# Performance work log

Measured on AMD Instinct MI355X. Metric: run time of the kernel, lower is better.

Reference implementation:

```python
import jax, jax.numpy as jnp
import numpy as np

LMAX, MMAX = 6, 2
C, COUT = 128, 128
M_SIZE = [LMAX - m + 1 for m in range(MMAX + 1)]  # [7, 6, 5]
LN_EPS = 1e-5


def _perm():
    # l-primary layout (input): for l in 0..lmax, m in -min(l,mmax)..min(l,mmax)
    lp = [(l, m) for l in range(LMAX + 1) for m in range(-min(l, MMAX), min(l, MMAX) + 1)]
    # m-primary layout (CoefficientMapping.to_m): m=0 block, then per m: real(+m) block, imag(-m) block
    mp = [(l, 0) for l in range(LMAX + 1)]
    for m in range(1, MMAX + 1):
        mp += [(l, m) for l in range(m, LMAX + 1)]
        mp += [(l, -m) for l in range(m, LMAX + 1)]
    return np.array([lp.index(t) for t in mp], dtype=np.int32)

PERM = _perm()  # length 29


def setup_inputs() -> dict:
    key = jax.random.key(0)
    ks = jax.random.split(key, 8)
    E = 30000
    num_coeff = sum(2 * min(l, MMAX) + 1 for l in range(LMAX + 1))  # 29
    rad_out = C * sum(M_SIZE)  # 2304 = num_channels_rad
    s = 0.02
    return {
        "x_emb": jax.random.normal(ks[0], (E, num_coeff, C), jnp.float32),
        "x_edge": jax.random.normal(ks[1], (E, C), jnp.float32),
        # RadialFunction: Linear(C,C)+LN+SiLU, Linear(C, rad_out)
        "rad_w1": jax.random.normal(ks[2], (C, C), jnp.float32) * s,
        "rad_b1": jnp.zeros((C,), jnp.float32),
        "rad_g": jnp.ones((C,), jnp.float32),
        "rad_beta": jnp.zeros((C,), jnp.float32),
        "rad_w2": jax.random.normal(ks[3], (rad_out, C), jnp.float32) * s,
        "rad_b2": jnp.ones((rad_out,), jnp.float32),  # gate ~1 so signal survives
        # fc_m0: Linear(7*C, COUT*7, bias=True)
        "w_m0": jax.random.normal(ks[4], (M_SIZE[0] * COUT, M_SIZE[0] * C), jnp.float32) * s,
        "b_m0": jnp.zeros((M_SIZE[0] * COUT,), jnp.float32),
        # SO2_m_Convolution fc for m=1,2: Linear(msz*C, 2*COUT*msz, bias=False)
        "w_m1": jax.random.normal(ks[5], (2 * COUT * M_SIZE[1], M_SIZE[1] * C), jnp.float32) * s,
        "w_m2": jax.random.normal(ks[6], (2 * COUT * M_SIZE[2], M_SIZE[2] * C), jnp.float32) * s,
    }


def reference(x_emb, x_edge, rad_w1, rad_b1, rad_g, rad_beta, rad_w2, rad_b2,
              w_m0, b_m0, w_m1, w_m2):
    E = x_emb.shape[0]
    # _m_primary: permute coefficients from l-primary to m-primary layout
    xm = x_emb[:, PERM, :]  # (E, 29, C)

    # RadialFunction: Linear + LayerNorm + SiLU + Linear
    h = x_edge @ rad_w1.T + rad_b1
    mu = jnp.mean(h, axis=-1, keepdims=True)
    var = jnp.var(h, axis=-1, keepdims=True)
    h = (h - mu) * jax.lax.rsqrt(var + LN_EPS) * rad_g + rad_beta
    h = jax.nn.silu(h)
    rad = h @ rad_w2.T + rad_b2  # (E, 2304)

    # m = 0
    m0 = M_SIZE[0]
    x0 = xm[:, :m0, :].reshape(E, m0 * C)
    x0 = x0 * rad[:, : m0 * C]
    x0 = x0 @ w_m0.T + b_m0  # (E, m0*COUT)
    outs = [x0.reshape(E, m0, COUT)]

    offset, offr = m0, m0 * C
    for msz, w in zip(M_SIZE[1:], (w_m1, w_m2)):
        # (E, 2, msz*C): row 0 = real(+m) coeffs, row 1 = imag(-m) coeffs
        x_m = xm[:, offset:offset + 2 * msz, :].reshape(E, 2, msz * C)
        x_m = x_m * rad[:, offr:offr + msz * C][:, None, :]
        y = jnp.einsum('eki,oi->eko', x_m, w)  # (E, 2, 2*COUT*msz)
        half = w.shape[0] // 2
        y_r, y_i = y[..., :half], y[..., half:]
        out_r = y_r[:, 0:1] - y_i[:, 1:2]
        out_i = y_r[:, 1:2] + y_i[:, 0:1]
        outs.append(jnp.concatenate([out_r, out_i], axis=1).reshape(E, 2 * msz, COUT))
        offset += 2 * msz
        offr += msz * C

    return jnp.concatenate(outs, axis=1)  # (E, 29, COUT), m-primary layout
```

## Files before the change

kernel.cpp:

```cpp
#include <hip/hip_runtime.h>
#include <stdint.h>

typedef unsigned short u16;
typedef __attribute__((ext_vector_type(8))) short short8;
typedef __attribute__((ext_vector_type(8))) u16 u16x8;
typedef __attribute__((ext_vector_type(4))) u16 u16x4;
typedef __attribute__((ext_vector_type(4))) float f32x4;

#define E_TOT 30000
#define TL    3712

__constant__ int d_PERM[29] = {0,2,6,11,16,21,26, 3,7,12,17,22,27, 1,5,10,15,20,25,
                               8,13,18,23,28, 4,9,14,19,24};
__constant__ int d_RINV[18][2] = {
  {0,-1},{1,-1},{2,-1},{3,-1},{4,-1},{5,-1},{6,-1},
  {7,13},{8,14},{9,15},{10,16},{11,17},{12,18},
  {19,24},{20,25},{21,26},{22,27},{23,28}};

__device__ __forceinline__ u16 f2bf(float f){
  union { float f; uint32_t u; } v; v.f = f;
  return (u16)((v.u + 0x7FFFu + ((v.u >> 16) & 1u)) >> 16);
}
__device__ __forceinline__ float bf2f(u16 u){
  union { uint32_t u; float f; } v; v.u = ((uint32_t)u) << 16;
  return v.f;
}
__device__ __forceinline__ void gl_lds16(const void* g, void* l){
  __builtin_amdgcn_global_load_lds((const __attribute__((address_space(1))) void*)g,
                                   (__attribute__((address_space(3))) void*)l, 16, 0, 0);
}

__global__ void k_build_w(const float* __restrict__ w0, const float* __restrict__ w1,
                          const float* __restrict__ w2, const float* __restrict__ rw2,
                          u16* __restrict__ W0, u16* __restrict__ W1, u16* __restrict__ W2,
                          u16* __restrict__ w2b){
  int idx = blockIdx.x * 256 + threadIdx.x;
  if (idx < 2304*128){ w2b[idx] = f2bf(rw2[idx]); return; }
  idx -= 2304*128;
  if (idx < 1024*896){
    W0[idx] = (idx < 896*896) ? f2bf(w0[idx]) : (u16)0;
    return;
  }
  idx -= 1024*896;
  if (idx < 1536*1536){
    const int half = 768;
    int o = idx / 1536, i2 = idx - o*1536;
    float v;
    if (o < half) v = (i2 < half) ? w1[o*half + i2] : -w1[(half+o)*half + (i2-half)];
    else { int op = o - half;
           v = (i2 < half) ? w1[(half+op)*half + i2] : w1[op*half + (i2-half)]; }
    W1[idx] = f2bf(v);
    return;
  }
  idx -= 1536*1536;
  if (idx < 1280*1280){
    const int half = 640;
    int o = idx / 1280, i2 = idx - o*1280;
    float v;
    if (o < half) v = (i2 < half) ? w2[o*half + i2] : -w2[(half+o)*half + (i2-half)];
    else { int op = o - half;
           v = (i2 < half) ? w2[(half+op)*half + i2] : w2[op*half + (i2-half)]; }
    W2[idx] = f2bf(v);
  }
}

__global__ __launch_bounds__(256) void k_h(const float* __restrict__ xe,
    const float* __restrict__ w1, const float* __restrict__ b1,
    const float* __restrict__ g, const float* __restrict__ beta,
    u16* __restrict__ hout){
  __shared__ float sw[128*132];
  __shared__ float sxe[16*128];
  int tid = threadIdx.x;
  #pragma unroll
  for (int q = 0; q < 16; q++){
    int i4 = q*256 + tid;
    int row = i4 >> 5, c4 = (i4 & 31) * 4;
    *(f32x4*)&sw[row*132 + c4] = *(const f32x4*)&w1[row*128 + c4];
  }
  int el = tid >> 4, s = tid & 15;
  for (int g8 = 0; g8 < 8; g8++){
    long eb = (long)blockIdx.x * 128 + g8*16;
    if (eb >= E_TOT) break;
    __syncthreads();
    #pragma unroll
    for (int q = 0; q < 2; q++){
      int off = q*1024 + tid*4;
      long er = eb + (off >> 7); if (er > (long)(E_TOT-1)) er = (long)(E_TOT-1);
      *(f32x4*)&sxe[off] = *(const f32x4*)&xe[er*128 + (off & 127)];
    }
    __syncthreads();
    float acc[8];
    #pragma unroll
    for (int q = 0; q < 8; q++) acc[q] = 0.f;
    const float* xr = &sxe[el*128];
    for (int c4 = 0; c4 < 32; c4++){
      f32x4 x = *(const f32x4*)&xr[c4*4];
      #pragma unroll
      for (int q = 0; q < 8; q++){
        f32x4 w = *(const f32x4*)&sw[(s + 16*q)*132 + c4*4];
        acc[q] += x[0]*w[0] + x[1]*w[1] + x[2]*w[2] + x[3]*w[3];
      }
    }
    float sum = 0.f, ss = 0.f;
    #pragma unroll
    for (int q = 0; q < 8; q++){
      acc[q] += b1[s + 16*q];
      sum += acc[q]; ss += acc[q]*acc[q];
    }
    #pragma unroll
    for (int m = 1; m < 16; m <<= 1){ sum += __shfl_xor(sum, m); ss += __shfl_xor(ss, m); }
    float mu = sum * (1.f/128.f);
    float var = ss * (1.f/128.f) - mu*mu;
    float rs = rsqrtf(var + 1e-5f);
    long e = eb + el;
    if (e < (long)E_TOT){
      #pragma unroll
      for (int q = 0; q < 8; q++){
        int j = s + 16*q;
        float v = (acc[q] - mu) * rs * g[j] + beta[j];
        v = v / (1.f + expf(-v));
        hout[e*128 + j] = f2bf(v);
      }
    }
  }
}

__global__ __launch_bounds__(256) void k_radt(
    const u16* __restrict__ h, const u16* __restrict__ w2b,
    const float* __restrict__ b2, const float* __restrict__ xemb,
    u16* __restrict__ t)
{
  __shared__ u16 sH[64*136];
  __shared__ u16 sT[64*72];
  int tid = threadIdx.x;
  long eb = (long)blockIdx.x * 64;
  int nn0 = blockIdx.y * 9;
  #pragma unroll
  for (int q = 0; q < 4; q++){
    int ch = q*256 + tid;
    int row = ch >> 4, col = (ch & 15) * 8;
    long er = eb + row; if (er > (long)(E_TOT-1)) er = (long)(E_TOT-1);
    *(u16x8*)&sH[row*136 + col] = *(const u16x8*)&h[er*128 + col];
  }
  __syncthreads();
  int lane = tid & 63, wid = tid >> 6;
  int wr = wid >> 1, wc = wid & 1;
  int lr = lane & 15, lh = lane >> 4;
  short8 afr[2][4];
  #pragma unroll
  for (int mi = 0; mi < 2; mi++)
    #pragma unroll
    for (int ks = 0; ks < 4; ks++)
      afr[mi][ks] = *(const short8*)&sH[(wr*32 + mi*16 + lr)*136 + ks*32 + lh*8];

  for (int nn = nn0; nn < nn0 + 9; ++nn){
    int nb = nn * 64;
    f32x4 acc[2][2];
    #pragma unroll
    for (int mi = 0; mi < 2; mi++)
      #pragma unroll
      for (int nj = 0; nj < 2; nj++){ acc[mi][nj][0]=0;acc[mi][nj][1]=0;acc[mi][nj][2]=0;acc[mi][nj][3]=0; }
    #pragma unroll
    for (int ks = 0; ks < 4; ks++){
      #pragma unroll
      for (int nj = 0; nj < 2; nj++){
        short8 bf = *(const short8*)&w2b[(long)(nb + wc*32 + nj*16 + lr)*128 + ks*32 + lh*8];
        #pragma unroll
        for (int mi = 0; mi < 2; mi++)
          acc[mi][nj] = __builtin_amdgcn_mfma_f32_16x16x32_bf16(afr[mi][ks], bf, acc[mi][nj], 0, 0, 0);
      }
    }
    __syncthreads();
    #pragma unroll
    for (int mi = 0; mi < 2; mi++){
      #pragma unroll
      for (int nj = 0; nj < 2; nj++){
        int col = wc*32 + nj*16 + lr;
        float bv = b2[nb + col];
        #pragma unroll
        for (int q = 0; q < 4; q++){
          int row = wr*32 + mi*16 + lh*4 + q;
          sT[row*72 + col] = f2bf(acc[mi][nj][q] + bv);
        }
      }
    }
    __syncthreads();
    int rcb = nb >> 7, chalf = nb & 64;
    #pragma unroll
    for (int rr = 0; rr < 2; rr++){
      int r = d_RINV[rcb][rr];
      if (r < 0) break;
      int xrow = d_PERM[r];
      #pragma unroll
      for (int q = 0; q < 2; q++){
        int ch = q*256 + tid;
        int row = ch >> 3, c8 = (ch & 7) * 8;
        long e = eb + row;
        if (e < (long)E_TOT){
          const float* xp = &xemb[(e*29 + xrow)*128 + chalf + c8];
          f32x4 x0 = *(const f32x4*)xp;
          f32x4 x1 = *(const f32x4*)(xp + 4);
          u16x8 rv = *(const u16x8*)&sT[row*72 + c8];
          u16x8 o;
          o[0]=f2bf(x0[0]*bf2f(rv[0])); o[1]=f2bf(x0[1]*bf2f(rv[1]));
          o[2]=f2bf(x0[2]*bf2f(rv[2])); o[3]=f2bf(x0[3]*bf2f(rv[3]));
          o[4]=f2bf(x1[0]*bf2f(rv[4])); o[5]=f2bf(x1[1]*bf2f(rv[5]));
          o[6]=f2bf(x1[2]*bf2f(rv[6])); o[7]=f2bf(x1[3]*bf2f(rv[7]));
          *(u16x8*)&t[(e*29 + r)*128 + chalf + c8] = o;
        }
      }
    }
  }
}

__global__ __launch_bounds__(256, 4) void k_gemm(
    const u16* __restrict__ A,
    const u16* __restrict__ W0c, const u16* __restrict__ W1c, const u16* __restrict__ W2c,
    const float* __restrict__ bias0, float* __restrict__ out)
{
  __shared__ u16 SA[128*64];
  __shared__ u16 SB[128*64];

  int orig = blockIdx.x;
  int xcd = orig & 7, idx = orig >> 3;
  int wgid = (xcd < 7 ? xcd*852 : 5964) + idx;

  int mi_ = wgid / 29, nidx = wgid - mi_*29;
  int mrow = mi_ * 128;
  int K, kbase, ncol; const u16* Wg; const float* bias = nullptr;
  if (nidx < 7)       { K=896;  kbase=0;    Wg=W0c; ncol=nidx*128;      bias=bias0; }
  else if (nidx < 19) { K=1536; kbase=896;  Wg=W1c; ncol=(nidx-7)*128;  }
  else                { K=1280; kbase=2432; Wg=W2c; ncol=(nidx-19)*128; }
  int nkt = K >> 6;

  int tid = threadIdx.x;
  int lane = tid & 63, wid = tid >> 6;
  int wr = wid >> 1, wc = wid & 1;
  int lr = lane & 15, lh = lane >> 4;
  int swz = (lane & 7) << 3;

  const u16* gA[4]; const u16* gB[4]; int oS[4];
  #pragma unroll
  for (int q = 0; q < 4; q++){
    int CH = q*256 + tid;
    int row = CH >> 3, c16 = CH & 7;
    int cs = (c16 ^ (row & 7)) << 3;
    long e = mrow + row; if (e > (long)(E_TOT-1)) e = (long)(E_TOT-1);
    gA[q] = A + e*(long)TL + kbase + cs;
    gB[q] = Wg + (long)(ncol + row)*K + cs;
    oS[q] = CH * 8;
  }

  f32x4 acc[4][4];
  #pragma unroll
  for (int i = 0; i < 4; i++)
    #pragma unroll
    for (int j = 0; j < 4; j++){ acc[i][j][0]=0;acc[i][j][1]=0;acc[i][j][2]=0;acc[i][j][3]=0; }

  for (int t = 0; t < nkt; ++t){
    if (t) __syncthreads();
    #pragma unroll
    for (int q = 0; q < 4; q++){ gl_lds16(gA[q], &SA[oS[q]]); gA[q] += 64; }
    #pragma unroll
    for (int q = 0; q < 4; q++){ gl_lds16(gB[q], &SB[oS[q]]); gB[q] += 64; }
    __syncthreads();
    #pragma unroll
    for (int ks = 0; ks < 2; ks++){
      short8 a[4], b[4];
      #pragma unroll
      for (int i = 0; i < 4; i++)
        a[i] = *(const short8*)&SA[(wr*64 + i*16 + lr)*64 + ((ks*32 + lh*8) ^ swz)];
      #pragma unroll
      for (int j = 0; j < 4; j++)
        b[j] = *(const short8*)&SB[(wc*64 + j*16 + lr)*64 + ((ks*32 + lh*8) ^ swz)];
      #pragma unroll
      for (int i = 0; i < 4; i++)
        #pragma unroll
        for (int j = 0; j < 4; j++)
          acc[i][j] = __builtin_amdgcn_mfma_f32_16x16x32_bf16(a[i], b[j], acc[i][j], 0, 0, 0);
    }
  }

  #pragma unroll
  for (int i = 0; i < 4; i++){
    #pragma unroll
    for (int j = 0; j < 4; j++){
      int lc = ncol + wc*64 + j*16 + lr;
      float bv = bias ? bias[lc] : 0.f;
      #pragma unroll
      for (int q = 0; q < 4; q++){
        long row = mrow + wr*64 + i*16 + lh*4 + q;
        if (row < E_TOT)
          out[row*(long)TL + kbase + lc] = acc[i][j][q] + bv;
      }
    }
  }
}

extern "C" void kernel_launch(void* const* d_in, const int* in_sizes, int n_in,
                              void* d_out, int out_size, void* d_ws, size_t ws_size,
                              hipStream_t stream){
  (void)in_sizes; (void)n_in; (void)out_size;
  const float* x_emb  = (const float*)d_in[0];
  const float* x_edge = (const float*)d_in[1];
  const float* rad_w1 = (const float*)d_in[2];
  const float* rad_b1 = (const float*)d_in[3];
  const float* rad_g  = (const float*)d_in[4];
  const float* rad_bt = (const float*)d_in[5];
  const float* rad_w2 = (const float*)d_in[6];
  const float* rad_b2 = (const float*)d_in[7];
  const float* w_m0   = (const float*)d_in[8];
  const float* b_m0   = (const float*)d_in[9];
  const float* w_m1   = (const float*)d_in[10];
  const float* w_m2   = (const float*)d_in[11];
  float* out = (float*)d_out;
  char* ws = (char*)d_ws;

  u16* t   = (u16*)(ws + 0);
  u16* h   = (u16*)(ws + 222720000);
  u16* W0  = (u16*)(ws + 230400000);
  u16* W1  = (u16*)(ws + 232235008);
  u16* W2  = (u16*)(ws + 236953600);
  u16* w2b = (u16*)(ws + 240230400);
  if (ws_size < 240820224ull) return;

  k_build_w<<<dim3(20352), dim3(256), 0, stream>>>(w_m0, w_m1, w_m2, rad_w2,
                                                   W0, W1, W2, w2b);
  k_h<<<dim3(235), dim3(256), 0, stream>>>(x_edge, rad_w1, rad_b1, rad_g, rad_bt, h);
  k_radt<<<dim3(469, 4), dim3(256), 0, stream>>>(h, w2b, rad_b2, x_emb, t);
  k_gemm<<<dim3(6815), dim3(256), 0, stream>>>(t, W0, W1, W2, b_m0, out);
}
```

Before: 737.0 us.

## Enlarge GEMM tile to 256x128 with 8 waves; double-buffer radial staging

The main GEMM moves from 128x128 tiles with 4 waves to 256x128 tiles with 512 threads in a single shared buffer. Each weight tile loaded into LDS is now reused across twice as many edge rows, and the XCD-aware block remap is recomputed for the new grid. In k_radt, the staging buffer for the radial output is double-buffered and the x_emb loads are issued before the tile is written. This removes one barrier per iteration and hides global-load latency behind the MFMA and LDS work. In exchange there is more register pressure and LDS per block, and a coarser grid in which the last row tile is mostly padding.

Result: faster. 647.4 us (-12.2%).

```diff
diff --git a/kernel.cpp b/kernel.cpp
--- a/kernel.cpp
+++ b/kernel.cpp
@@ -131,7 +131,7 @@
     u16* __restrict__ t)
 {
   __shared__ u16 sH[64*136];
-  __shared__ u16 sT[64*72];
+  __shared__ u16 sT[2][64*72];
   int tid = threadIdx.x;
   long eb = (long)blockIdx.x * 64;
   int nn0 = blockIdx.y * 9;
@@ -154,6 +154,7 @@
       afr[mi][ks] = *(const short8*)&sH[(wr*32 + mi*16 + lr)*136 + ks*32 + lh*8];
 
   for (int nn = nn0; nn < nn0 + 9; ++nn){
+    int p = nn & 1;
     int nb = nn * 64;
     f32x4 acc[2][2];
     #pragma unroll
@@ -170,7 +171,26 @@
           acc[mi][nj] = __builtin_amdgcn_mfma_f32_16x16x32_bf16(afr[mi][ks], bf, acc[mi][nj], 0, 0, 0);
       }
     }
-    __syncthreads();
+    int rcb = nb >> 7, chalf = nb & 64;
+    int nr = (d_RINV[rcb][1] >= 0) ? 2 : 1;
+    f32x4 px0[2][2], px1[2][2];
+    #pragma unroll
+    for (int rr = 0; rr < 2; rr++){
+      if (rr < nr){
+        int xrow = d_PERM[d_RINV[rcb][rr]];
+        #pragma unroll
+        for (int q = 0; q < 2; q++){
+          int ch = q*256 + tid;
+          int row = ch >> 3, c8 = (ch & 7) * 8;
+          long e = eb + row;
+          if (e < (long)E_TOT){
+            const float* xp = &xemb[(e*29 + xrow)*128 + chalf + c8];
+            px0[rr][q] = *(const f32x4*)xp;
+            px1[rr][q] = *(const f32x4*)(xp + 4);
+          }
+        }
+      }
+    }
     #pragma unroll
     for (int mi = 0; mi < 2; mi++){
       #pragma unroll
@@ -180,57 +200,52 @@
         #pragma unroll
         for (int q = 0; q < 4; q++){
           int row = wr*32 + mi*16 + lh*4 + q;
-          sT[row*72 + col] = f2bf(acc[mi][nj][q] + bv);
+          sT[p][row*72 + col] = f2bf(acc[mi][nj][q] + bv);
         }
       }
     }
     __syncthreads();
-    int rcb = nb >> 7, chalf = nb & 64;
     #pragma unroll
     for (int rr = 0; rr < 2; rr++){
-      int r = d_RINV[rcb][rr];
-      if (r < 0) break;
-      int xrow = d_PERM[r];
-      #pragma unroll
-      for (int q = 0; q < 2; q++){
-        int ch = q*256 + tid;
-        int row = ch >> 3, c8 = (ch & 7) * 8;
-        long e = eb + row;
-        if (e < (long)E_TOT){
-          const float* xp = &xemb[(e*29 + xrow)*128 + chalf + c8];
-          f32x4 x0 = *(const f32x4*)xp;
-          f32x4 x1 = *(const f32x4*)(xp + 4);
-          u16x8 rv = *(const u16x8*)&sT[row*72 + c8];
-          u16x8 o;
-          o[0]=f2bf(x0[0]*bf2f(rv[0])); o[1]=f2bf(x0[1]*bf2f(rv[1]));
-          o[2]=f2bf(x0[2]*bf2f(rv[2])); o[3]=f2bf(x0[3]*bf2f(rv[3]));
-          o[4]=f2bf(x1[0]*bf2f(rv[4])); o[5]=f2bf(x1[1]*bf2f(rv[5]));
-          o[6]=f2bf(x1[2]*bf2f(rv[6])); o[7]=f2bf(x1[3]*bf2f(rv[7]));
-          *(u16x8*)&t[(e*29 + r)*128 + chalf + c8] = o;
+      if (rr < nr){
+        int r = d_RINV[rcb][rr];
+        #pragma unroll
+        for (int q = 0; q < 2; q++){
+          int ch = q*256 + tid;
+          int row = ch >> 3, c8 = (ch & 7) * 8;
+          long e = eb + row;
+          if (e < (long)E_TOT){
+            u16x8 rv = *(const u16x8*)&sT[p][row*72 + c8];
+            u16x8 o;
+            o[0]=f2bf(px0[rr][q][0]*bf2f(rv[0])); o[1]=f2bf(px0[rr][q][1]*bf2f(rv[1]));
+            o[2]=f2bf(px0[rr][q][2]*bf2f(rv[2])); o[3]=f2bf(px0[rr][q][3]*bf2f(rv[3]));
+            o[4]=f2bf(px1[rr][q][0]*bf2f(rv[4])); o[5]=f2bf(px1[rr][q][1]*bf2f(rv[5]));
+            o[6]=f2bf(px1[rr][q][2]*bf2f(rv[6])); o[7]=f2bf(px1[rr][q][3]*bf2f(rv[7]));
+            *(u16x8*)&t[(e*29 + r)*128 + chalf + c8] = o;
+          }
         }
       }
     }
   }
 }
 
-__global__ __launch_bounds__(256, 4) void k_gemm(
+__global__ __launch_bounds__(512, 4) void k_gemm(
     const u16* __restrict__ A,
     const u16* __restrict__ W0c, const u16* __restrict__ W1c, const u16* __restrict__ W2c,
     const float* __restrict__ bias0, float* __restrict__ out)
 {
-  __shared__ u16 SA[128*64];
-  __shared__ u16 SB[128*64];
+  __shared__ u16 S[24576];
 
   int orig = blockIdx.x;
-  int xcd = orig & 7, idx = orig >> 3;
-  int wgid = (xcd < 7 ? xcd*852 : 5964) + idx;
+  int xcd = orig & 7, idxs = orig >> 3;
+  int wgid = (xcd < 6 ? xcd*428 : 2568 + (xcd-6)*427) + idxs;
 
   int mi_ = wgid / 29, nidx = wgid - mi_*29;
-  int mrow = mi_ * 128;
-  int K, kbase, ncol; const u16* Wg; const float* bias = nullptr;
-  if (nidx < 7)       { K=896;  kbase=0;    Wg=W0c; ncol=nidx*128;      bias=bias0; }
-  else if (nidx < 19) { K=1536; kbase=896;  Wg=W1c; ncol=(nidx-7)*128;  }
-  else                { K=1280; kbase=2432; Wg=W2c; ncol=(nidx-19)*128; }
+  int mrow = mi_ * 256;
+  int K, kbase, ncol, nvalid; const u16* Wg; const float* bias = nullptr;
+  if (nidx < 12)      { K=1536; kbase=896;  Wg=W1c; ncol=nidx*128;      nvalid=1536; }
+  else if (nidx < 22) { K=1280; kbase=2432; Wg=W2c; ncol=(nidx-12)*128; nvalid=1280; }
+  else                { K=896;  kbase=0;    Wg=W0c; ncol=(nidx-22)*128; nvalid=896; bias=bias0; }
   int nkt = K >> 6;
 
   int tid = threadIdx.x;
@@ -239,16 +254,21 @@
   int lr = lane & 15, lh = lane >> 4;
   int swz = (lane & 7) << 3;
 
-  const u16* gA[4]; const u16* gB[4]; int oS[4];
+  const u16* gsrc[6]; int ldso[6];
   #pragma unroll
   for (int q = 0; q < 4; q++){
-    int CH = q*256 + tid;
+    int CH = q*512 + tid;
     int row = CH >> 3, c16 = CH & 7;
-    int cs = (c16 ^ (row & 7)) << 3;
     long e = mrow + row; if (e > (long)(E_TOT-1)) e = (long)(E_TOT-1);
-    gA[q] = A + e*(long)TL + kbase + cs;
-    gB[q] = Wg + (long)(ncol + row)*K + cs;
-    oS[q] = CH * 8;
+    gsrc[q] = A + e*(long)TL + kbase + ((c16 ^ (row & 7)) << 3);
+    ldso[q] = row*64 + c16*8;
+  }
+  #pragma unroll
+  for (int q = 0; q < 2; q++){
+    int CH = q*512 + tid;
+    int row = CH >> 3, c16 = CH & 7;
+    gsrc[4+q] = Wg + (long)(ncol + row)*K + ((c16 ^ (row & 7)) << 3);
+    ldso[4+q] = 16384 + row*64 + c16*8;
   }
 
   f32x4 acc[4][4];
@@ -260,24 +280,25 @@
   for (int t = 0; t < nkt; ++t){
     if (t) __syncthreads();
     #pragma unroll
-    for (int q = 0; q < 4; q++){ gl_lds16(gA[q], &SA[oS[q]]); gA[q] += 64; }
-    #pragma unroll
-    for (int q = 0; q < 4; q++){ gl_lds16(gB[q], &SB[oS[q]]); gB[q] += 64; }
+    for (int q = 0; q < 6; q++){ gl_lds16(gsrc[q], &S[ldso[q]]); gsrc[q] += 64; }
     __syncthreads();
-    #pragma unroll
-    for (int ks = 0; ks < 2; ks++){
-      short8 a[4], b[4];
-      #pragma unroll
-      for (int i = 0; i < 4; i++)
-        a[i] = *(const short8*)&SA[(wr*64 + i*16 + lr)*64 + ((ks*32 + lh*8) ^ swz)];
-      #pragma unroll
-      for (int j = 0; j < 4; j++)
-        b[j] = *(const short8*)&SB[(wc*64 + j*16 + lr)*64 + ((ks*32 + lh*8) ^ swz)];
-      #pragma unroll
-      for (int i = 0; i < 4; i++)
-        #pragma unroll
-        for (int j = 0; j < 4; j++)
-          acc[i][j] = __builtin_amdgcn_mfma_f32_16x16x32_bf16(a[i], b[j], acc[i][j], 0, 0, 0);
+    short8 af[4][2];
+    #pragma unroll
+    for (int i = 0; i < 4; i++)
+      #pragma unroll
+      for (int ks = 0; ks < 2; ks++)
+        af[i][ks] = *(const short8*)&S[(wr*64 + i*16 + lr)*64 + ((ks*32 + lh*8) ^ swz)];
+    #pragma unroll
+    for (int nj = 0; nj < 4; nj++){
+      short8 bf[2];
+      #pragma unroll
+      for (int ks = 0; ks < 2; ks++)
+        bf[ks] = *(const short8*)&S[16384 + (wc*64 + nj*16 + lr)*64 + ((ks*32 + lh*8) ^ swz)];
+      #pragma unroll
+      for (int ks = 0; ks < 2; ks++)
+        #pragma unroll
+        for (int i = 0; i < 4; i++)
+          acc[i][nj] = __builtin_amdgcn_mfma_f32_16x16x32_bf16(af[i][ks], bf[ks], acc[i][nj], 0, 0, 0);
     }
   }
 
@@ -285,13 +306,15 @@
   for (int i = 0; i < 4; i++){
     #pragma unroll
     for (int j = 0; j < 4; j++){
-      int lc = ncol + wc*64 + j*16 + lr;
-      float bv = bias ? bias[lc] : 0.f;
-      #pragma unroll
-      for (int q = 0; q < 4; q++){
-        long row = mrow + wr*64 + i*16 + lh*4 + q;
-        if (row < E_TOT)
-          out[row*(long)TL + kbase + lc] = acc[i][j][q] + bv;
+      int col = wc*64 + j*16 + lr;
+      if (ncol + col < nvalid){
+        float bv = bias ? bias[ncol + col] : 0.f;
+        #pragma unroll
+        for (int q = 0; q < 4; q++){
+          long row = mrow + wr*64 + i*16 + lh*4 + q;
+          if (row < E_TOT)
+            out[row*(long)TL + kbase + ncol + col] = acc[i][j][q] + bv;
+        }
       }
     }
   }
@@ -328,5 +351,5 @@
                                                    W0, W1, W2, w2b);
   k_h<<<dim3(235), dim3(256), 0, stream>>>(x_edge, rad_w1, rad_b1, rad_g, rad_bt, h);
   k_radt<<<dim3(469, 4), dim3(256), 0, stream>>>(h, w2b, rad_b2, x_emb, t);
-  k_gemm<<<dim3(6815), dim3(256), 0, stream>>>(t, W0, W1, W2, b_m0, out);
-}
+  k_gemm<<<dim3(3422), dim3(512), 0, stream>>>(t, W0, W1, W2, b_m0, out);
+}
```
